# Kernel tuning notes

Hardware: AMD Instinct MI355X
Metric: run time of the kernel (lower is better)

The kernel has to match this reference:

```python
import jax, jax.numpy as jnp
import numpy as np


def _local_indices(H, W, K):
    # KxK local window per pixel; border neighbors clamped to the image (replicate padding)
    half = K // 2
    d = np.arange(-half, half + 1)
    r = np.clip(np.arange(H)[:, None, None, None] + d[None, None, :, None], 0, H - 1)
    c = np.clip(np.arange(W)[None, :, None, None] + d[None, None, None, :], 0, W - 1)
    return (r * W + c).reshape(H * W, K * K).astype(np.int32)


def setup_inputs():
    B, C, H, W = 2, 32, 128, 128
    K, S = 25, 1024
    N = H * W
    k1, k2, k3, k4 = jax.random.split(jax.random.key(0), 4)
    key_feat = jax.random.normal(k1, (B, C, H, W), dtype=jnp.float32)
    query_feat = jax.random.normal(k2, (B, C, H, W), dtype=jnp.float32)
    segment_target = jax.random.randint(k3, (B, 1, H, W), 0, 64, dtype=jnp.int32)
    local = jnp.broadcast_to(jnp.asarray(_local_indices(H, W, K))[None], (B, N, K * K))
    rand_glob = jax.random.randint(k4, (B, N, S - K * K), 0, N, dtype=jnp.int32)
    sample_inds = jnp.concatenate([local, rand_glob], axis=-1)  # [B, N, S]
    return {"key_feat": key_feat, "query_feat": query_feat,
            "segment_target": segment_target, "sample_inds": sample_inds}


def _affinity_logits(key_f, query_f, sample_inds, chunk=1024):
    # key_f, query_f: [B, N, C]; sample_inds: [B, N, S]
    B, N, C = key_f.shape
    S = sample_inds.shape[-1]
    nchunks = N // chunk
    q_c = query_f.reshape(B, nchunks, chunk, C).transpose(1, 0, 2, 3)
    i_c = sample_inds.reshape(B, nchunks, chunk, S).transpose(1, 0, 2, 3)

    def body(carry, args):
        q, idx = args                                   # [B, chunk, C], [B, chunk, S]
        kg = jax.vmap(lambda kb, ib: kb[ib])(key_f, idx)  # [B, chunk, S, C]
        return carry, jnp.einsum('bnsc,bnc->bns', kg, q)

    _, lc = jax.lax.scan(body, None, (q_c, i_c))        # [nchunks, B, chunk, S]
    logits = lc.transpose(1, 0, 2, 3).reshape(B, N, S)
    return logits * (C ** -0.5)


def _loss(logits, sample_inds, segment_target):
    B, N, S = logits.shape
    seg = segment_target.reshape(B, N)
    samples = jax.vmap(lambda s, i: s[i])(seg, sample_inds)      # [B, N, S]
    targets = (seg[:, :, None] == samples).astype(logits.dtype)
    mask = (seg != 0).astype(logits.dtype)[:, :, None]           # [B, N, 1]
    # weighted_softmax(logits, mask)
    xe = jnp.exp(logits - jnp.max(logits, -1, keepdims=True))
    denom = jnp.sum(xe * mask, -1, keepdims=True)
    y_prob = xe * mask / (denom + 1e-9)
    y_pred = jnp.log(jnp.clip(y_prob, 1e-8, None))
    y_true = targets / (jnp.sum(targets, -1, keepdims=True) + 1e-9)
    # F.kl_div(y_pred, y_true, reduction='none') with 0*log(0) = 0
    kl = jnp.where(y_true > 0,
                   y_true * (jnp.log(jnp.clip(y_true, 1e-30, None)) - y_pred),
                   0.0) * mask
    agg_mask = (jnp.sum(mask, -1) > 0).astype(logits.dtype)
    return jnp.sum(kl) / (jnp.sum(agg_mask) + 1e-9)


def reference(key_feat, query_feat, segment_target, sample_inds):
    B, C, H, W = key_feat.shape
    N = H * W
    key_f = key_feat.reshape(B, C, N).transpose(0, 2, 1)    # [B, N, C]
    query_f = query_feat.reshape(B, C, N).transpose(0, 2, 1)
    logits = _affinity_logits(key_f, query_f, sample_inds)  # [B, N, S], scaled by C**-0.5
    loss = _loss(logits, sample_inds, segment_target)
    return (logits, loss)
```

## Files before the change

### kernel.cpp

```cpp
#include <hip/hip_runtime.h>
#include <stdint.h>

typedef _Float16 h2 __attribute__((ext_vector_type(2)));
typedef _Float16 h4 __attribute__((ext_vector_type(4)));
typedef float    f4 __attribute__((ext_vector_type(4)));

static constexpr int CDIM = 32;
static constexpr int NPIX = 16384;
static constexpr int SSAM = 1024;
static constexpr int ROWS_PER_BLOCK = 16;

__device__ __forceinline__ uint16_t f2h(float f) {
    union { _Float16 h; uint16_t u; } c;
    c.h = (_Float16)f;
    return c.u;
}

template<int CTRL>
__device__ __forceinline__ float dpp_add(float x) {
    int y = __builtin_amdgcn_mov_dpp(__float_as_int(x), CTRL, 0xF, 0xF, true);
    return x + __int_as_float(y);
}

__device__ __forceinline__ float dot2(h2 a, h2 b, float c) {
    return __builtin_amdgcn_fdot2(a, b, c, false);
}

__global__ __launch_bounds__(256)
void prep_kernel(const float* __restrict__ key_f,
                 const float* __restrict__ query_f,
                 const int* __restrict__ seg32,
                 uint8_t* __restrict__ key16,
                 uint8_t* __restrict__ q16,
                 uint8_t* __restrict__ seg8,
                 uint32_t* __restrict__ segbit,
                 int N, int rows, float scale)
{
    int gI = blockIdx.x * 256 + threadIdx.x;
    if (gI >= rows) return;
    segbit[2 * gI]     = 0;
    segbit[2 * gI + 1] = 0;
    seg8[gI] = (uint8_t)seg32[gI];

    int b = gI / N, n = gI - b * N;
    const size_t cb = (size_t)b * CDIM;

    uint32_t kp[16], qp[16];
#pragma unroll
    for (int c = 0; c < CDIM; c += 2) {
        float k0 = key_f[(cb + c) * N + n];
        float k1 = key_f[(cb + c + 1) * N + n];
        float q0 = query_f[(cb + c) * N + n] * scale;
        float q1 = query_f[(cb + c + 1) * N + n] * scale;
        kp[c >> 1] = (uint32_t)f2h(k0) | ((uint32_t)f2h(k1) << 16);
        qp[c >> 1] = (uint32_t)f2h(q0) | ((uint32_t)f2h(q1) << 16);
    }
    uint4* ko = (uint4*)(key16 + ((size_t)gI << 6));
    uint4* qo = (uint4*)(q16 + ((size_t)gI << 6));
#pragma unroll
    for (int j = 0; j < 4; ++j) {
        ko[j] = make_uint4(kp[4*j], kp[4*j+1], kp[4*j+2], kp[4*j+3]);
        qo[j] = make_uint4(qp[4*j], qp[4*j+1], qp[4*j+2], qp[4*j+3]);
    }
}

__global__ __launch_bounds__(256)
void segbit_build(const int* __restrict__ seg32,
                  uint32_t* __restrict__ segbit,
                  int N, int rows)
{
    int g = blockIdx.x * 256 + threadIdx.x;
    if (g >= rows) return;
    int b = g / N, n = g - b * N;
    int v = seg32[g] & 63;
    atomicOr(&segbit[(((size_t)(b * 64 + v)) << 9) + (n >> 5)], 1u << (n & 31));
}

__global__ __launch_bounds__(256)
void dense_local(const uint8_t* __restrict__ key16,
                 const uint8_t* __restrict__ q16,
                 const uint8_t* __restrict__ seg8,
                 float* __restrict__ out,
                 float* __restrict__ zA,
                 float* __restrict__ tA,
                 float* __restrict__ slA)
{
    const int tid  = threadIdx.x;
    const int bid  = blockIdx.x;
    const int b    = bid >> 8;
    const int t8   = bid & 255;
    const int y0   = (t8 >> 4) << 3;
    const int x0   = (t8 & 15) << 3;
    const int lane = tid & 63;
    const int w    = tid >> 6;

    __shared__ __align__(16) uint8_t kslot[256 * 80];
    __shared__ __align__(16) float   res[4][16][256];
    __shared__ uint8_t wseg[1024];
    __shared__ float   rowacc[4][16][3];

    const uint8_t* kb = key16 + ((size_t)b << 20);
    const uint8_t* sb = seg8 + ((size_t)b << 14);
    const int yo = y0 - 12, xo = x0 - 12;

    for (int s = tid; s < 1024; s += 256) {
        int i = s >> 5, j = s & 31;
        int yy = min(max(yo + i, 0), 127);
        int xx = min(max(xo + j, 0), 127);
        wseg[s] = sb[(yy << 7) + xx];
    }
    if (tid < 192) ((float*)rowacc)[tid] = 0.f;

    const int qsel = (w << 4) + (lane & 15);
    const int qyA  = qsel >> 3, qxA = qsel & 7;
    const size_t qrow = ((size_t)b << 14) + ((size_t)(y0 + qyA) << 7) + (x0 + qxA);
    const int koff = (lane >> 4) << 3;
    const h4 a0 = *(const h4*)(q16 + (qrow << 6) + koff);
    const h4 a1 = *(const h4*)(q16 + (qrow << 6) + 32 + koff);

    __syncthreads();

    for (int t = 0; t < 4; ++t) {
        for (int s = tid; s < 1024; s += 256) {
            int slot = s >> 2, q = s & 3;
            int i = (t << 3) + (slot >> 5), j = slot & 31;
            int yy = min(max(yo + i, 0), 127);
            int xx = min(max(xo + j, 0), 127);
            *(uint4*)(kslot + slot * 80 + (q << 4)) =
                *(const uint4*)(kb + ((((size_t)(yy << 7)) + xx) << 6) + (q << 4));
        }
        __syncthreads();

#pragma unroll 4
        for (int n = 0; n < 16; ++n) {
            const uint8_t* kr = kslot + ((n << 4) + (lane & 15)) * 80;
            h4 b0 = *(const h4*)(kr + koff);
            h4 b1 = *(const h4*)(kr + 32 + koff);
            f4 acc = {0.f, 0.f, 0.f, 0.f};
            acc = __builtin_amdgcn_mfma_f32_16x16x16f16(a0, b0, acc, 0, 0, 0);
            acc = __builtin_amdgcn_mfma_f32_16x16x16f16(a1, b1, acc, 0, 0, 0);
#pragma unroll
            for (int r = 0; r < 4; ++r)
                res[w][((lane >> 4) << 2) + r][(n << 4) + (lane & 15)] = acc[r];
        }

        for (int m = 0; m < 16; ++m) {
            const int q  = (w << 4) + m;
            const int qy = q >> 3, qx = q & 7;
            const int row = (b << 14) + ((y0 + qy) << 7) + (x0 + qx);
            const int segr = (int)wseg[((qy + 12) << 5) + qx + 12];
            int sLo = ((t << 3) - qy) * 25; if (sLo < 0) sLo = 0;
            int sHi = ((t << 3) - qy + 8) * 25; if (sHi > 512) sHi = 512;
            float z = 0.f, tc = 0.f, sl = 0.f;
            for (int s = sLo + lane; s < sHi; s += 64) {
                int d25 = (s * 5243) >> 17;
                int r25 = s - d25 * 25;
                int i  = qy + d25;
                int wc = qx + r25;
                float v = res[w][m][((i - (t << 3)) << 5) + wc];
                out[((size_t)row << 10) + s] = v;
                z += __expf(v);
                if ((int)wseg[(i << 5) + wc] == segr) { tc += 1.f; sl += v; }
            }
#pragma unroll
            for (int off = 32; off >= 1; off >>= 1) {
                z  += __shfl_xor(z,  off, 64);
                tc += __shfl_xor(tc, off, 64);
                sl += __shfl_xor(sl, off, 64);
            }
            if (lane == 0) {
                rowacc[w][m][0] += z;
                rowacc[w][m][1] += tc;
                rowacc[w][m][2] += sl;
            }
        }
        __syncthreads();
    }

    if (tid < 64) {
        int q = tid, qy = q >> 3, qx = q & 7;
        int row = (b << 14) + ((y0 + qy) << 7) + (x0 + qx);
        zA[row]  = rowacc[q >> 4][q & 15][0];
        tA[row]  = rowacc[q >> 4][q & 15][1];
        slA[row] = rowacc[q >> 4][q & 15][2];
    }
}

__global__ __launch_bounds__(256)
void affinity_rand(const int* __restrict__ inds,
                   const uint8_t* __restrict__ key16,
                   const uint8_t* __restrict__ q16,
                   const int* __restrict__ seg32,
                   const uint32_t* __restrict__ segbit,
                   const float* __restrict__ zA,
                   const float* __restrict__ tA,
                   const float* __restrict__ slA,
                   float* __restrict__ out,
                   float* __restrict__ ws_kl)
{
    const int tid  = threadIdx.x;
    const int row0 = blockIdx.x * ROWS_PER_BLOCK;
    const int b    = row0 >> 14;
    const int lane = tid & 63;
    const int w    = tid >> 6;
    const int g    = lane >> 2;
    const int sub  = lane & 3;

    __shared__ __align__(16) int      idx_lds[2][512];
    __shared__ __align__(16) uint32_t bm_lds[2][512];
    __shared__ float red[2][3][4];
    __shared__ float zp[ROWS_PER_BLOCK], tp[ROWS_PER_BLOCK], sp[ROWS_PER_BLOCK];

    const uint32_t* sbase_bm = segbit + ((size_t)(b * 64) << 9);

    if (tid < ROWS_PER_BLOCK)      zp[tid] = zA[row0 + tid];
    else if (tid < 2*ROWS_PER_BLOCK) tp[tid - ROWS_PER_BLOCK] = tA[row0 + tid - ROWS_PER_BLOCK];
    else if (tid < 3*ROWS_PER_BLOCK) sp[tid - 2*ROWS_PER_BLOCK] = slA[row0 + tid - 2*ROWS_PER_BLOCK];

    ((int2*)idx_lds[0])[tid] =
        ((const int2*)(inds + ((size_t)row0 << 10) + 512))[tid];
    int scur = seg32[row0];
    ((uint2*)bm_lds[0])[tid] =
        ((const uint2*)(sbase_bm + ((size_t)(scur & 63) << 9)))[tid];
    uint4 qcur = *(const uint4*)(q16 + ((size_t)row0 << 6) + (sub << 4));
    __syncthreads();

    const uint8_t* kb = key16 + ((size_t)b << 20);
    const uint32_t subs = (uint32_t)(sub << 4);
    const int sbase = (w << 7) + g;

    for (int r = 0; r < ROWS_PER_BLOCK; ++r) {
        const int row = row0 + r;
        const int p   = r & 1;
        const int* cur = idx_lds[p];
        const bool hasNext = (r + 1 < ROWS_PER_BLOCK);

        h2 qh0, qh1, qh2, qh3;
        {
            union { uint4 u; h2 h[4]; } qc; qc.u = qcur;
            qh0 = qc.h[0]; qh1 = qc.h[1]; qh2 = qc.h[2]; qh3 = qc.h[3];
        }
        const int seg_n = scur;

        int idxs[8];
#pragma unroll
        for (int i = 0; i < 8; ++i)
            idxs[i] = cur[sbase + (i << 4)];

        uint4 kd[8];
#pragma unroll
        for (int i = 0; i < 8; ++i)
            kd[i] = *(const uint4*)(kb + (((uint32_t)idxs[i] << 6) | subs));

        int2 pre; uint4 qnext; uint2 pre_bm; int snext;
        if (hasNext) {
            pre    = ((const int2*)(inds + ((size_t)(row + 1) << 10) + 512))[tid];
            qnext  = *(const uint4*)(q16 + ((size_t)(row + 1) << 6) + (sub << 4));
            snext  = seg32[row + 1];
            pre_bm = ((const uint2*)(sbase_bm + ((size_t)(snext & 63) << 9)))[tid];
        }
        int tfm = 0;
#pragma unroll
        for (int j = 0; j < 2; ++j) {
            int idx = cur[sbase + (((j << 2) | sub) << 4)];
            if ((bm_lds[p][idx >> 5] >> (idx & 31)) & 1u) tfm |= 1 << j;
        }

        float lg0 = 0.f, lg1 = 0.f;
#pragma unroll
        for (int i = 0; i < 8; ++i) {
            union { uint4 u; h2 h[4]; } kc; kc.u = kd[i];
            float acc = dot2(kc.h[0], qh0, 0.f);
            acc = dot2(kc.h[1], qh1, acc);
            acc = dot2(kc.h[2], qh2, acc);
            acc = dot2(kc.h[3], qh3, acc);
            acc = dpp_add<0xB1>(acc);
            acc = dpp_add<0x4E>(acc);
            if (sub == (i & 3)) {
                if ((i >> 2) == 0) lg0 = acc;
                else               lg1 = acc;
            }
        }

        const size_t rowbase = (size_t)row << 10;
        float* op = out + rowbase + 512 + (w << 7) + (sub << 4) + g;
        op[0]  = lg0;
        op[64] = lg1;

        float z  = __expf(lg0) + __expf(lg1);
        float tc = (float)__popc((unsigned)tfm);
        float sl = 0.f;
        sl += (tfm & 1) ? lg0 : 0.f;
        sl += (tfm & 2) ? lg1 : 0.f;
#pragma unroll
        for (int off = 32; off >= 1; off >>= 1) {
            z  += __shfl_xor(z,  off, 64);
            tc += __shfl_xor(tc, off, 64);
            sl += __shfl_xor(sl, off, 64);
        }
        if (lane == 0) {
            red[p][0][w] = z;
            red[p][1][w] = tc;
            red[p][2][w] = sl;
        }

        if (hasNext) {
            ((int2*)idx_lds[p ^ 1])[tid] = pre;
            ((uint2*)bm_lds[p ^ 1])[tid] = pre_bm;
            qcur = qnext;
            scur = snext;
        }
        __syncthreads();

        if (tid == 0) {
            if (seg_n != 0) {
                const float Z  = zp[r] + (red[p][0][0] + red[p][0][1]) + (red[p][0][2] + red[p][0][3]);
                const float T  = tp[r] + (red[p][1][0] + red[p][1][1]) + (red[p][1][2] + red[p][1][3]);
                const float SL = sp[r] + (red[p][2][0] + red[p][2][1]) + (red[p][2][2] + red[p][2][3]);
                ws_kl[row] = -__logf(T) - SL / T + __logf(Z);
            } else {
                ws_kl[row] = 0.f;
            }
        }
    }
}

__global__ __launch_bounds__(256)
void affinity_fallback(const float* __restrict__ key_f,
                       const float* __restrict__ query_f,
                       const int*   __restrict__ seg32,
                       const int*   __restrict__ inds,
                       float* __restrict__ out,
                       float* __restrict__ ws_kl,
                       int N, int S, float scale)
{
    const int bid = blockIdx.x;
    const int tid = threadIdx.x;
    const int b   = bid / N;

    __shared__ float q_lds[CDIM];
    __shared__ float redA[4], redB[4], redC[4];

    if (tid < CDIM) {
        int n = bid - b * N;
        q_lds[tid] = query_f[((size_t)(b * CDIM + tid)) * N + n];
    }
    const int seg_n = seg32[bid];
    __syncthreads();

    float q[CDIM];
#pragma unroll
    for (int c = 0; c < CDIM; ++c) q[c] = q_lds[c];

    const size_t rowbase = (size_t)bid * S;
    const int4 iv = ((const int4*)(inds + rowbase))[tid];
    const int idxv[4] = {iv.x, iv.y, iv.z, iv.w};

    float lg[4];
    int   tf[4];
#pragma unroll
    for (int k = 0; k < 4; ++k) {
        int idx = idxv[k];
        tf[k] = (seg32[b * N + idx] == seg_n) ? 1 : 0;
        float acc = 0.f;
#pragma unroll
        for (int c = 0; c < CDIM; ++c)
            acc = fmaf(key_f[((size_t)(b * CDIM + c)) * N + idx], q[c], acc);
        lg[k] = acc * scale;
    }
    ((float4*)(out + rowbase))[tid] = make_float4(lg[0], lg[1], lg[2], lg[3]);

    const int lane = tid & 63, wv = tid >> 6;
    float m = fmaxf(fmaxf(lg[0], lg[1]), fmaxf(lg[2], lg[3]));
#pragma unroll
    for (int off = 32; off >= 1; off >>= 1)
        m = fmaxf(m, __shfl_xor(m, off, 64));
    if (lane == 0) redA[wv] = m;
    __syncthreads();
    m = fmaxf(fmaxf(redA[0], redA[1]), fmaxf(redA[2], redA[3]));

    float e[4], z = 0.f, tcnt = 0.f;
#pragma unroll
    for (int k = 0; k < 4; ++k) {
        e[k] = expf(lg[k] - m);
        z += e[k];
        tcnt += (float)tf[k];
    }
#pragma unroll
    for (int off = 32; off >= 1; off >>= 1) {
        z    += __shfl_xor(z, off, 64);
        tcnt += __shfl_xor(tcnt, off, 64);
    }
    if (lane == 0) { redB[wv] = z; redC[wv] = tcnt; }
    __syncthreads();
    const float Z = redB[0] + redB[1] + redB[2] + redB[3];
    const float T = redC[0] + redC[1] + redC[2] + redC[3];

    float kl = 0.f;
    if (seg_n != 0) {
        const float invZ = 1.f / (Z + 1e-9f);
        const float invT = 1.f / (T + 1e-9f);
        const float nlT  = -logf(T + 1e-9f);
#pragma unroll
        for (int k = 0; k < 4; ++k) {
            if (tf[k]) {
                float p = e[k] * invZ;
                float yp = logf(fmaxf(p, 1e-8f));
                kl += invT * (nlT - yp);
            }
        }
    }
#pragma unroll
    for (int off = 32; off >= 1; off >>= 1)
        kl += __shfl_xor(kl, off, 64);
    if (lane == 0) redA[wv] = kl;
    __syncthreads();
    if (tid == 0)
        ws_kl[bid] = redA[0] + redA[1] + redA[2] + redA[3];
}

__global__ __launch_bounds__(1024)
void loss_reduce(const float* __restrict__ ws_kl,
                 const int* __restrict__ seg32,
                 float* __restrict__ out_loss, int rows)
{
    const int tid = threadIdx.x;
    float s = 0.f, c = 0.f;
    for (int i = tid; i < rows; i += 1024) {
        s += ws_kl[i];
        c += (seg32[i] != 0) ? 1.f : 0.f;
    }
#pragma unroll
    for (int off = 32; off >= 1; off >>= 1) {
        s += __shfl_xor(s, off, 64);
        c += __shfl_xor(c, off, 64);
    }
    __shared__ float sA[16], sB[16];
    const int lane = tid & 63, wv = tid >> 6;
    if (lane == 0) { sA[wv] = s; sB[wv] = c; }
    __syncthreads();
    if (tid == 0) {
        float ts = 0.f, tc = 0.f;
#pragma unroll
        for (int k = 0; k < 16; ++k) { ts += sA[k]; tc += sB[k]; }
        out_loss[0] = ts / (tc + 1e-9f);
    }
}

extern "C" void kernel_launch(void* const* d_in, const int* in_sizes, int n_in,
                              void* d_out, int out_size, void* d_ws, size_t ws_size,
                              hipStream_t stream)
{
    const float* key_f   = (const float*)d_in[0];
    const float* query_f = (const float*)d_in[1];
    const int*   seg32   = (const int*)d_in[2];
    const int*   inds    = (const int*)d_in[3];
    float* out = (float*)d_out;

    const int N    = NPIX;
    const int rows = in_sizes[2];
    const int S    = in_sizes[3] / rows;
    const float scale = (float)(1.0 / sqrt((double)CDIM));
    const int B    = rows / N;

    const size_t off_q16 = (size_t)rows * 64;
    const size_t off_s8  = off_q16 + (size_t)rows * 64;
    const size_t off_sb  = (off_s8 + (size_t)rows + 255) & ~(size_t)255;
    const size_t sb_words = (size_t)B * 64 * 512;
    const size_t off_zA  = (off_sb + sb_words * 4 + 255) & ~(size_t)255;
    const size_t off_tA  = off_zA + (size_t)rows * 4;
    const size_t off_slA = off_tA + (size_t)rows * 4;
    const size_t off_kl  = off_slA + (size_t)rows * 4;
    const size_t need    = off_kl + (size_t)rows * 4;

    uint8_t* wsb = (uint8_t*)d_ws;
    const bool geom_ok = (S == SSAM) && (rows % N == 0) &&
                         (rows % ROWS_PER_BLOCK == 0);

    if (ws_size >= need && geom_ok) {
        uint8_t*  key16  = wsb;
        uint8_t*  q16    = wsb + off_q16;
        uint8_t*  seg8   = wsb + off_s8;
        uint32_t* segbit = (uint32_t*)(wsb + off_sb);
        float*    zA     = (float*)(wsb + off_zA);
        float*    tA     = (float*)(wsb + off_tA);
        float*    slA    = (float*)(wsb + off_slA);
        float*    wskl   = (float*)(wsb + off_kl);

        prep_kernel<<<(rows + 255) / 256, 256, 0, stream>>>(
            key_f, query_f, seg32, key16, q16, seg8, segbit, N, rows, scale);
        segbit_build<<<(rows + 255) / 256, 256, 0, stream>>>(
            seg32, segbit, N, rows);
        dense_local<<<B * 256, 256, 0, stream>>>(
            key16, q16, seg8, out, zA, tA, slA);
        affinity_rand<<<rows / ROWS_PER_BLOCK, 256, 0, stream>>>(
            inds, key16, q16, seg32, segbit, zA, tA, slA, out, wskl);
        loss_reduce<<<1, 1024, 0, stream>>>(wskl, seg32, out + (size_t)rows * S, rows);
    } else {
        float* wskl = (float*)d_ws;
        affinity_fallback<<<rows, 256, 0, stream>>>(
            key_f, query_f, seg32, inds, out, wskl, N, S, scale);
        loss_reduce<<<1, 1024, 0, stream>>>(wskl, seg32, out + (size_t)rows * S, rows);
    }
}
```

Measured before the change: 203.1 us.

## Compute all 625 local-window logits densely and store MFMA results as fp16

The dense local-window kernel now covers the full 25x25 window (625 samples) instead of the first 512. The random-sample gather kernel only handles the remaining 399 indices, so its thread-to-sample mapping is re-indexed and guarded for the partial last slot. The MFMA result buffer in shared memory changes from float to half, halving its footprint so more blocks may fit per CU. The cost is lower precision in the stored local logits, plus extra predication and uneven work in the gather path.

```diff
diff --git a/kernel.cpp b/kernel.cpp
--- a/kernel.cpp
+++ b/kernel.cpp
@@ -8,6 +8,8 @@
 static constexpr int CDIM = 32;
 static constexpr int NPIX = 16384;
 static constexpr int SSAM = 1024;
+static constexpr int NLOC = 625;
+static constexpr int NRND = SSAM - NLOC;
 static constexpr int ROWS_PER_BLOCK = 16;
 
 __device__ __forceinline__ uint16_t f2h(float f) {
@@ -94,8 +96,8 @@
     const int lane = tid & 63;
     const int w    = tid >> 6;
 
-    __shared__ __align__(16) uint8_t kslot[256 * 80];
-    __shared__ __align__(16) float   res[4][16][256];
+    __shared__ __align__(16) uint8_t  kslot[256 * 80];
+    __shared__ __align__(16) _Float16 res[4][16][256];
     __shared__ uint8_t wseg[1024];
     __shared__ float   rowacc[4][16][3];
 
@@ -141,7 +143,8 @@
             acc = __builtin_amdgcn_mfma_f32_16x16x16f16(a1, b1, acc, 0, 0, 0);
 #pragma unroll
             for (int r = 0; r < 4; ++r)
-                res[w][((lane >> 4) << 2) + r][(n << 4) + (lane & 15)] = acc[r];
+                res[w][((lane >> 4) << 2) + r][(n << 4) + (lane & 15)] =
+                    (_Float16)acc[r];
         }
 
         for (int m = 0; m < 16; ++m) {
@@ -150,14 +153,14 @@
             const int row = (b << 14) + ((y0 + qy) << 7) + (x0 + qx);
             const int segr = (int)wseg[((qy + 12) << 5) + qx + 12];
             int sLo = ((t << 3) - qy) * 25; if (sLo < 0) sLo = 0;
-            int sHi = ((t << 3) - qy + 8) * 25; if (sHi > 512) sHi = 512;
+            int sHi = ((t << 3) - qy + 8) * 25; if (sHi > NLOC) sHi = NLOC;
             float z = 0.f, tc = 0.f, sl = 0.f;
             for (int s = sLo + lane; s < sHi; s += 64) {
                 int d25 = (s * 5243) >> 17;
                 int r25 = s - d25 * 25;
                 int i  = qy + d25;
                 int wc = qx + r25;
-                float v = res[w][m][((i - (t << 3)) << 5) + wc];
+                float v = (float)res[w][m][((i - (t << 3)) << 5) + wc];
                 out[((size_t)row << 10) + s] = v;
                 z += __expf(v);
                 if ((int)wseg[(i << 5) + wc] == segr) { tc += 1.f; sl += v; }
@@ -205,20 +208,24 @@
     const int w    = tid >> 6;
     const int g    = lane >> 2;
     const int sub  = lane & 3;
-
-    __shared__ __align__(16) int      idx_lds[2][512];
+    const int gidx = (w << 4) + g;
+
+    __shared__ __align__(16) int      idx_lds[2][448];
     __shared__ __align__(16) uint32_t bm_lds[2][512];
     __shared__ float red[2][3][4];
     __shared__ float zp[ROWS_PER_BLOCK], tp[ROWS_PER_BLOCK], sp[ROWS_PER_BLOCK];
 
     const uint32_t* sbase_bm = segbit + ((size_t)(b * 64) << 9);
 
-    if (tid < ROWS_PER_BLOCK)      zp[tid] = zA[row0 + tid];
-    else if (tid < 2*ROWS_PER_BLOCK) tp[tid - ROWS_PER_BLOCK] = tA[row0 + tid - ROWS_PER_BLOCK];
-    else if (tid < 3*ROWS_PER_BLOCK) sp[tid - 2*ROWS_PER_BLOCK] = slA[row0 + tid - 2*ROWS_PER_BLOCK];
-
-    ((int2*)idx_lds[0])[tid] =
-        ((const int2*)(inds + ((size_t)row0 << 10) + 512))[tid];
+    if (tid < ROWS_PER_BLOCK)           zp[tid] = zA[row0 + tid];
+    else if (tid < 2*ROWS_PER_BLOCK)    tp[tid - ROWS_PER_BLOCK] = tA[row0 + tid - ROWS_PER_BLOCK];
+    else if (tid < 3*ROWS_PER_BLOCK)    sp[tid - 2*ROWS_PER_BLOCK] = slA[row0 + tid - 2*ROWS_PER_BLOCK];
+
+    {
+        const int* ib = inds + ((size_t)row0 << 10) + NLOC;
+        idx_lds[0][tid] = ib[tid];
+        if (tid < NRND - 256) idx_lds[0][256 + tid] = ib[256 + tid];
+    }
     int scur = seg32[row0];
     ((uint2*)bm_lds[0])[tid] =
         ((const uint2*)(sbase_bm + ((size_t)(scur & 63) << 9)))[tid];
@@ -227,7 +234,7 @@
 
     const uint8_t* kb = key16 + ((size_t)b << 20);
     const uint32_t subs = (uint32_t)(sub << 4);
-    const int sbase = (w << 7) + g;
+    const bool act6 = (384 + gidx) < NRND;
 
     for (int r = 0; r < ROWS_PER_BLOCK; ++r) {
         const int row = row0 + r;
@@ -242,56 +249,62 @@
         }
         const int seg_n = scur;
 
-        int idxs[8];
-#pragma unroll
-        for (int i = 0; i < 8; ++i)
-            idxs[i] = cur[sbase + (i << 4)];
-
-        uint4 kd[8];
-#pragma unroll
-        for (int i = 0; i < 8; ++i)
+        int idxs[7];
+#pragma unroll
+        for (int i = 0; i < 7; ++i)
+            idxs[i] = cur[(i << 6) + gidx];
+
+        uint4 kd[7];
+#pragma unroll
+        for (int i = 0; i < 6; ++i)
             kd[i] = *(const uint4*)(kb + (((uint32_t)idxs[i] << 6) | subs));
-
-        int2 pre; uint4 qnext; uint2 pre_bm; int snext;
+        kd[6] = make_uint4(0, 0, 0, 0);
+        if (act6)
+            kd[6] = *(const uint4*)(kb + (((uint32_t)idxs[6] << 6) | subs));
+
+        int pre0 = 0, pre1 = 0; uint4 qnext; uint2 pre_bm; int snext;
         if (hasNext) {
-            pre    = ((const int2*)(inds + ((size_t)(row + 1) << 10) + 512))[tid];
+            const int* ib = inds + ((size_t)(row + 1) << 10) + NLOC;
+            pre0 = ib[tid];
+            if (tid < NRND - 256) pre1 = ib[256 + tid];
             qnext  = *(const uint4*)(q16 + ((size_t)(row + 1) << 6) + (sub << 4));
             snext  = seg32[row + 1];
             pre_bm = ((const uint2*)(sbase_bm + ((size_t)(snext & 63) << 9)))[tid];
         }
+        const bool owned1 = (sub < 2) || (sub == 2 && act6);
         int tfm = 0;
-#pragma unroll
-        for (int j = 0; j < 2; ++j) {
-            int idx = cur[sbase + (((j << 2) | sub) << 4)];
-            if ((bm_lds[p][idx >> 5] >> (idx & 31)) & 1u) tfm |= 1 << j;
-        }
-
+        {
+            int idx0 = cur[(sub << 6) + gidx];
+            if ((bm_lds[p][idx0 >> 5] >> (idx0 & 31)) & 1u) tfm |= 1;
+            if (sub < 3) {
+                int idx1 = cur[((sub + 4) << 6) + gidx];
+                if (owned1 && ((bm_lds[p][idx1 >> 5] >> (idx1 & 31)) & 1u))
+                    tfm |= 2;
+            }
+        }
+
+        const size_t obase = ((size_t)row << 10) + NLOC;
         float lg0 = 0.f, lg1 = 0.f;
 #pragma unroll
-        for (int i = 0; i < 8; ++i) {
-            union { uint4 u; h2 h[4]; } kc; kc.u = kd[i];
+        for (int it = 0; it < 7; ++it) {
+            union { uint4 u; h2 h[4]; } kc; kc.u = kd[it];
             float acc = dot2(kc.h[0], qh0, 0.f);
             acc = dot2(kc.h[1], qh1, acc);
             acc = dot2(kc.h[2], qh2, acc);
             acc = dot2(kc.h[3], qh3, acc);
             acc = dpp_add<0xB1>(acc);
             acc = dpp_add<0x4E>(acc);
-            if (sub == (i & 3)) {
-                if ((i >> 2) == 0) lg0 = acc;
-                else               lg1 = acc;
-            }
-        }
-
-        const size_t rowbase = (size_t)row << 10;
-        float* op = out + rowbase + 512 + (w << 7) + (sub << 4) + g;
-        op[0]  = lg0;
-        op[64] = lg1;
-
-        float z  = __expf(lg0) + __expf(lg1);
+            if (sub == (it & 3)) {
+                if (it < 4) lg0 = acc;
+                else        lg1 = acc;
+                if (it < 6 || act6)
+                    out[obase + (it << 6) + gidx] = acc;
+            }
+        }
+
+        float z  = __expf(lg0) + (owned1 ? __expf(lg1) : 0.f);
         float tc = (float)__popc((unsigned)tfm);
-        float sl = 0.f;
-        sl += (tfm & 1) ? lg0 : 0.f;
-        sl += (tfm & 2) ? lg1 : 0.f;
+        float sl = ((tfm & 1) ? lg0 : 0.f) + ((tfm & 2) ? lg1 : 0.f);
 #pragma unroll
         for (int off = 32; off >= 1; off >>= 1) {
             z  += __shfl_xor(z,  off, 64);
@@ -305,7 +318,8 @@
         }
 
         if (hasNext) {
-            ((int2*)idx_lds[p ^ 1])[tid] = pre;
+            idx_lds[p ^ 1][tid] = pre0;
+            if (tid < NRND - 256) idx_lds[p ^ 1][256 + tid] = pre1;
             ((uint2*)bm_lds[p ^ 1])[tid] = pre_bm;
             qcur = qnext;
             scur = snext;
```

Result: faster. 165.6 us (-18.4%).
